# Optimization experiments

Hardware: AMD Instinct MI355X
Metric: run time of the kernel (lower is better)

## Reference

```python
import jax, jax.numpy as jnp
import numpy as np

ALPHA = 0.15
KSIZE = 5
EPS = 1e-6


def _minmax_norm(x):
    # x: [B,1,H,W]; per-sample min-max normalize, 0.5 if nearly constant
    mn = x.min(axis=(1, 2, 3), keepdims=True)
    mx = x.max(axis=(1, 2, 3), keepdims=True)
    denom = mx - mn
    safe = jnp.where(denom > EPS, denom, 1.0)
    return jnp.where(denom > EPS, (x - mn) / safe, 0.5)


def _saliency_map(images, out_hw):
    # grayscale via luma weights
    w = jnp.array([0.299, 0.587, 0.114], dtype=images.dtype).reshape(1, 3, 1, 1)
    gray = (images * w).sum(axis=1, keepdims=True)  # [B,1,H,W]
    kernel = jnp.ones((1, 1, KSIZE, KSIZE), dtype=gray.dtype) / (KSIZE * KSIZE)
    dn = ('NCHW', 'OIHW', 'NCHW')
    local_mean = jax.lax.conv_general_dilated(gray, kernel, (1, 1), 'SAME', dimension_numbers=dn)
    local_mean_sq = jax.lax.conv_general_dilated(gray ** 2, kernel, (1, 1), 'SAME', dimension_numbers=dn)
    local_var = jnp.maximum(local_mean_sq - local_mean ** 2, 0.0)
    sal = _minmax_norm(local_var)
    if sal.shape[-2:] != out_hw:
        sal = jax.image.resize(sal, (sal.shape[0], 1, out_hw[0], out_hw[1]), method='bilinear')
    return jax.lax.stop_gradient(sal)  # computed under no_grad / detached in torch


def setup_inputs() -> dict:
    key = jax.random.key(0)
    k1, k2 = jax.random.split(key)
    features = jax.random.normal(k1, (64, 512, 28, 28), dtype=jnp.float32)
    images = jax.random.uniform(k2, (64, 3, 224, 224), dtype=jnp.float32)
    return {"features": features, "images": images}


def reference(features, images):
    sal = _saliency_map(images, features.shape[-2:])  # [B,1,Hf,Wf]
    attn = jnp.sqrt((features ** 2).mean(axis=1, keepdims=True))  # [B,1,Hf,Wf]
    attn = _minmax_norm(attn)
    loss = jnp.mean((attn - sal) ** 2)
    return ALPHA * loss
```

## Files before the change

### kernel.cpp

```cpp
#include <hip/hip_runtime.h>
#include <math.h>

#define BATCH 64
#define HIMG 224
#define WIMG 224
#define IMGPLANE (HIMG*WIMG)
#define CF 512
#define HF 28
#define WF 28
#define POS (HF*WF)
#define ALPHA_C 0.15f
#define EPS_C 1e-6f

#define STRIPS 14
#define SROWS 16
#define GROWS 20
#define GCOLS 228
#define GSTR 229
#define VSTR 261
#define SHN 4580

#define NATTN 512
#define NVARH (STRIPS*BATCH)

#define OFF_HRES 0
#define HRES_CNT (BATCH*HIMG*WF)
#define OFF_BMM (OFF_HRES + HRES_CNT)
#define OFF_AP  (OFF_BMM + BATCH*STRIPS*2)
#define OFF_ACC (OFF_AP + 8*BATCH*POS)
#define OFF_CNT (OFF_ACC + 1)

__global__ __launch_bounds__(256) void fat_k(const float* __restrict__ img,
                                             const float* __restrict__ f,
                                             float* __restrict__ ws) {
    __shared__ float sh[SHN];
    __shared__ float wred[8];
    int bid = blockIdx.x;
    int tid = threadIdx.x;
    int g11 = bid / 11, r11 = bid - 11 * g11;

    if (r11 < 4) {
        int ab = g11 * 4 + r11;
        if (ab == 0 && tid == 0) {
            ws[OFF_ACC] = 0.0f;
            ((unsigned*)ws)[OFF_CNT] = 0u;
        }
        if (tid >= 196) return;
        int b = ab >> 3, z = ab & 7;
        const float* fp = f + (size_t)(b * CF + z * 64) * POS + 4 * tid;
        float ax = 0.0f, ay = 0.0f, az = 0.0f, aw = 0.0f;
        #pragma unroll 8
        for (int c = 0; c < 64; c++) {
            float4 u = *(const float4*)(fp + (size_t)c * POS);
            ax += u.x * u.x; ay += u.y * u.y; az += u.z * u.z; aw += u.w * u.w;
        }
        float4 o = make_float4(ax, ay, az, aw);
        *(float4*)(ws + OFF_AP + (size_t)(z * BATCH + b) * POS + 4 * tid) = o;
        return;
    }

    int vb = g11 * 7 + (r11 - 4);
    int b = vb / STRIPS, sy = vb - b * STRIPS;
    int y0 = sy * SROWS;
    const float* imb = img + (size_t)b * 3 * IMGPLANE;

    for (int i = tid; i < GROWS * 56; i += 256) {
        int gr = i / 56, q = i - gr * 56;
        int gy = y0 - 2 + gr;
        float gx0 = 0.0f, gx1 = 0.0f, gx2 = 0.0f, gx3 = 0.0f;
        if ((unsigned)gy < HIMG) {
            const float* row = imb + gy * WIMG + 4 * q;
            float4 a = *(const float4*)(row);
            float4 bb = *(const float4*)(row + IMGPLANE);
            float4 c = *(const float4*)(row + 2 * IMGPLANE);
            gx0 = 0.299f * a.x + 0.587f * bb.x + 0.114f * c.x;
            gx1 = 0.299f * a.y + 0.587f * bb.y + 0.114f * c.y;
            gx2 = 0.299f * a.z + 0.587f * bb.z + 0.114f * c.z;
            gx3 = 0.299f * a.w + 0.587f * bb.w + 0.114f * c.w;
        }
        int base = gr * GSTR + 2 + 4 * q;
        sh[base] = gx0; sh[base + 1] = gx1; sh[base + 2] = gx2; sh[base + 3] = gx3;
    }
    if (tid < GROWS * 4) {
        int gr = tid >> 2, p = tid & 3;
        int gc = (p < 2) ? p : (224 + p);
        sh[gr * GSTR + gc] = 0.0f;
    }
    __syncthreads();

    int r = tid >> 4, s = tid & 15;
    int x0 = 14 * s;
    const float* gr0 = sh + r * GSTR;
    float c1[5], c2[5], vreg[14];
    #pragma unroll
    for (int m = 0; m < 5; m++) {
        float a = 0.0f, a2 = 0.0f;
        #pragma unroll
        for (int k = 0; k < 5; k++) {
            float u = gr0[k * GSTR + x0 + m];
            a += u; a2 += u * u;
        }
        c1[m] = a; c2[m] = a2;
    }
    float vmn = INFINITY, vmx = 0.0f;
    #pragma unroll
    for (int xi = 0; xi < 14; xi++) {
        int p = xi % 5;
        float s1 = c1[p], s2 = c2[p];
        #pragma unroll
        for (int m = 1; m < 5; m++) {
            s1 += c1[(p + m) % 5];
            s2 += c2[(p + m) % 5];
        }
        float m1 = s1 * 0.04f, m2 = s2 * 0.04f;
        float vv = fmaxf(m2 - m1 * m1, 0.0f);
        vreg[xi] = vv;
        vmn = fminf(vmn, vv); vmx = fmaxf(vmx, vv);
        if (xi < 13) {
            float a = 0.0f, a2 = 0.0f;
            #pragma unroll
            for (int k = 0; k < 5; k++) {
                float u = gr0[k * GSTR + x0 + xi + 5];
                a += u; a2 += u * u;
            }
            c1[p] = a; c2[p] = a2;
        }
    }
    #pragma unroll
    for (int o = 32; o > 0; o >>= 1) {
        vmn = fminf(vmn, __shfl_xor(vmn, o));
        vmx = fmaxf(vmx, __shfl_xor(vmx, o));
    }
    __syncthreads();
    int w = tid >> 6;
    if ((tid & 63) == 0) { wred[w] = vmn; wred[4 + w] = vmx; }
    if (tid < SROWS * 8) {
        int rr = tid >> 3, p = tid & 7;
        int jh = p + ((p < 4) ? 0 : 224);
        sh[rr * VSTR + jh + (jh >> 3)] = 0.0f;
    }
    #pragma unroll
    for (int xi = 0; xi < 14; xi++) {
        int jh = x0 + xi + 4;
        sh[r * VSTR + jh + (jh >> 3)] = vreg[xi];
    }
    __syncthreads();
    if (tid == 0) {
        float mn = fminf(fminf(wred[0], wred[1]), fminf(wred[2], wred[3]));
        float mx = fmaxf(fmaxf(wred[4], wred[5]), fmaxf(wred[6], wred[7]));
        int blk = b * STRIPS + sy;
        ws[OFF_BMM + 2 * blk]     = mn;
        ws[OFF_BMM + 2 * blk + 1] = mx;
    }

    float* hb = ws + OFF_HRES + ((size_t)b * HIMG + y0) * WF;
    for (int idx = tid; idx < SROWS * WF; idx += 256) {
        int rr = idx / WF, i = idx - rr * WF;
        float acc = 0.0f, wsum = 0.0f;
        int j0 = 8 * i - 4;
        #pragma unroll
        for (int t = 0; t < 16; t++) {
            int j = j0 + t;
            float w_ = 8.0f - fabsf((float)t - 7.5f);
            int jh = j + 4;
            acc += w_ * sh[rr * VSTR + jh + (jh >> 3)];
            if ((unsigned)j < WIMG) wsum += w_;
        }
        hb[idx] = acc / wsum;
    }
}

__global__ __launch_bounds__(256) void fused_k(float* __restrict__ ws,
                                               float* __restrict__ out) {
    __shared__ float hres[HIMG][WF + 1];
    __shared__ float wred[4];
    __shared__ float s_mn, s_mx;
    int b = blockIdx.x;
    int tid = threadIdx.x;

    if (tid < 64) {
        float mn = INFINITY, mx = 0.0f;
        if (tid < STRIPS) {
            mn = ws[OFF_BMM + 2 * (b * STRIPS + tid)];
            mx = ws[OFF_BMM + 2 * (b * STRIPS + tid) + 1];
        }
        #pragma unroll
        for (int o = 8; o > 0; o >>= 1) {
            mn = fminf(mn, __shfl_down(mn, o));
            mx = fmaxf(mx, __shfl_down(mx, o));
        }
        if (tid == 0) { s_mn = mn; s_mx = mx; }
    }

    const float* hg = ws + OFF_HRES + (size_t)b * HIMG * WF;
    for (int i = tid; i < HIMG * WF; i += 256) {
        int y = i / WF, x = i - y * WF;
        hres[y][x] = hg[i];
    }
    __syncthreads();

    float vmn = s_mn, vmx = s_mx;
    float vden = vmx - vmn;
    bool vok = vden > EPS_C;

    const float* ap = ws + OFF_AP + (size_t)b * POS;
    float salv[4], attnv[4];
    float amn = INFINITY, amx = -INFINITY;
    #pragma unroll
    for (int k = 0; k < 4; k++) {
        int idx = tid + 256 * k;
        salv[k] = 0.0f; attnv[k] = 0.0f;
        if (idx < POS) {
            int yo = idx / WF, x = idx - yo * WF;
            float acc = 0.0f, wsum = 0.0f;
            int j0 = 8 * yo - 4;
            #pragma unroll
            for (int t = 0; t < 16; t++) {
                int j = j0 + t;
                float w = 8.0f - fabsf((float)t - 7.5f);
                if ((unsigned)j < HIMG) { acc += w * hres[j][x]; wsum += w; }
            }
            float sraw = acc / wsum;
            salv[k] = vok ? (sraw - vmn) / vden : 0.5f;
            float ssum = 0.0f;
            #pragma unroll
            for (int z = 0; z < 8; z++)
                ssum += ap[(size_t)z * BATCH * POS + idx];
            float a = sqrtf(ssum * (1.0f / CF));
            attnv[k] = a;
            amn = fminf(amn, a); amx = fmaxf(amx, a);
        }
    }

    #pragma unroll
    for (int o = 32; o > 0; o >>= 1) {
        amn = fminf(amn, __shfl_xor(amn, o));
        amx = fmaxf(amx, __shfl_xor(amx, o));
    }
    int w = tid >> 6;
    if ((tid & 63) == 0) wred[w] = amn;
    __syncthreads();
    if (tid == 0) s_mn = fminf(fminf(wred[0], wred[1]), fminf(wred[2], wred[3]));
    __syncthreads();
    if ((tid & 63) == 0) wred[w] = amx;
    __syncthreads();
    if (tid == 0) s_mx = fmaxf(fmaxf(wred[0], wred[1]), fmaxf(wred[2], wred[3]));
    __syncthreads();
    amn = s_mn; amx = s_mx;
    float aden = amx - amn;
    bool aok = aden > EPS_C;

    float lsum = 0.0f;
    #pragma unroll
    for (int k = 0; k < 4; k++) {
        int idx = tid + 256 * k;
        if (idx < POS) {
            float an = aok ? (attnv[k] - amn) / aden : 0.5f;
            float d = an - salv[k];
            lsum += d * d;
        }
    }
    #pragma unroll
    for (int o = 32; o > 0; o >>= 1) lsum += __shfl_xor(lsum, o);
    if ((tid & 63) == 0) wred[w] = lsum;
    __syncthreads();

    if (tid == 0) {
        float part = wred[0] + wred[1] + wred[2] + wred[3];
        atomicAdd(ws + OFF_ACC, part);
        __threadfence();
        unsigned old = atomicAdd((unsigned*)ws + OFF_CNT, 1u);
        if (old == BATCH - 1) {
            float tot = atomicAdd(ws + OFF_ACC, 0.0f);
            out[0] = tot * (ALPHA_C / (float)(BATCH * POS));
        }
    }
}

extern "C" void kernel_launch(void* const* d_in, const int* in_sizes, int n_in,
                              void* d_out, int out_size, void* d_ws, size_t ws_size,
                              hipStream_t stream) {
    const float* features = (const float*)d_in[0];
    const float* images   = (const float*)d_in[1];
    float* ws  = (float*)d_ws;
    float* out = (float*)d_out;

    hipLaunchKernelGGL(fat_k,   dim3(NATTN + NVARH), dim3(256), 0, stream,
                       images, features, ws);
    hipLaunchKernelGGL(fused_k, dim3(BATCH),         dim3(256), 0, stream, ws, out);
}
```

Before: 191.8 us.

## Split fused attention/variance kernel into separate launches with finer channel split

Breaks the combined kernel, which interleaved attention-reduction blocks and image-variance blocks, into two separate kernels. The channel reduction now uses 16 groups of 32 channels instead of 8 groups of 64, which doubles the attention block count to 1024, and the final kernel sums 16 partials. The aim is simpler per-block indexing and more parallelism for the feature stream. The cost is an extra launch, loss of the overlap between the two workloads, and more partial-sum traffic.

After: 193.9 us. About the same (+1.1%).

```diff
diff --git a/kernel.cpp b/kernel.cpp
--- a/kernel.cpp
+++ b/kernel.cpp
@@ -15,52 +15,47 @@
 #define STRIPS 14
 #define SROWS 16
 #define GROWS 20
-#define GCOLS 228
 #define GSTR 229
 #define VSTR 261
 #define SHN 4580
 
-#define NATTN 512
-#define NVARH (STRIPS*BATCH)
+#define ZG 16
+#define ZCH 32
 
 #define OFF_HRES 0
 #define HRES_CNT (BATCH*HIMG*WF)
 #define OFF_BMM (OFF_HRES + HRES_CNT)
 #define OFF_AP  (OFF_BMM + BATCH*STRIPS*2)
-#define OFF_ACC (OFF_AP + 8*BATCH*POS)
+#define OFF_ACC (OFF_AP + ZG*BATCH*POS)
 #define OFF_CNT (OFF_ACC + 1)
 
-__global__ __launch_bounds__(256) void fat_k(const float* __restrict__ img,
-                                             const float* __restrict__ f,
-                                             float* __restrict__ ws) {
+__global__ __launch_bounds__(256) void attn_k(const float* __restrict__ f,
+                                              float* __restrict__ ws) {
+    int z = blockIdx.x, b = blockIdx.y;
+    int tid = threadIdx.x;
+    if (z == 0 && b == 0 && tid == 0) {
+        ws[OFF_ACC] = 0.0f;
+        ((unsigned*)ws)[OFF_CNT] = 0u;
+    }
+    if (tid >= 196) return;
+    const float* fp = f + (size_t)(b * CF + z * ZCH) * POS + 4 * tid;
+    float ax = 0.0f, ay = 0.0f, az = 0.0f, aw = 0.0f;
+    #pragma unroll
+    for (int c = 0; c < ZCH; c++) {
+        float4 u = *(const float4*)(fp + (size_t)c * POS);
+        ax += u.x * u.x; ay += u.y * u.y;
+        az += u.z * u.z; aw += u.w * u.w;
+    }
+    *(float4*)(ws + OFF_AP + (size_t)(z * BATCH + b) * POS + 4 * tid) =
+        make_float4(ax, ay, az, aw);
+}
+
+__global__ __launch_bounds__(256) void varh_k(const float* __restrict__ img,
+                                              float* __restrict__ ws) {
     __shared__ float sh[SHN];
     __shared__ float wred[8];
-    int bid = blockIdx.x;
+    int sy = blockIdx.x, b = blockIdx.y;
     int tid = threadIdx.x;
-    int g11 = bid / 11, r11 = bid - 11 * g11;
-
-    if (r11 < 4) {
-        int ab = g11 * 4 + r11;
-        if (ab == 0 && tid == 0) {
-            ws[OFF_ACC] = 0.0f;
-            ((unsigned*)ws)[OFF_CNT] = 0u;
-        }
-        if (tid >= 196) return;
-        int b = ab >> 3, z = ab & 7;
-        const float* fp = f + (size_t)(b * CF + z * 64) * POS + 4 * tid;
-        float ax = 0.0f, ay = 0.0f, az = 0.0f, aw = 0.0f;
-        #pragma unroll 8
-        for (int c = 0; c < 64; c++) {
-            float4 u = *(const float4*)(fp + (size_t)c * POS);
-            ax += u.x * u.x; ay += u.y * u.y; az += u.z * u.z; aw += u.w * u.w;
-        }
-        float4 o = make_float4(ax, ay, az, aw);
-        *(float4*)(ws + OFF_AP + (size_t)(z * BATCH + b) * POS + 4 * tid) = o;
-        return;
-    }
-
-    int vb = g11 * 7 + (r11 - 4);
-    int b = vb / STRIPS, sy = vb - b * STRIPS;
     int y0 = sy * SROWS;
     const float* imb = img + (size_t)b * 3 * IMGPLANE;
 
@@ -224,7 +219,7 @@
             salv[k] = vok ? (sraw - vmn) / vden : 0.5f;
             float ssum = 0.0f;
             #pragma unroll
-            for (int z = 0; z < 8; z++)
+            for (int z = 0; z < ZG; z++)
                 ssum += ap[(size_t)z * BATCH * POS + idx];
             float a = sqrtf(ssum * (1.0f / CF));
             attnv[k] = a;
@@ -285,7 +280,7 @@
     float* ws  = (float*)d_ws;
     float* out = (float*)d_out;
 
-    hipLaunchKernelGGL(fat_k,   dim3(NATTN + NVARH), dim3(256), 0, stream,
-                       images, features, ws);
+    hipLaunchKernelGGL(attn_k,  dim3(ZG, BATCH),     dim3(256), 0, stream, features, ws);
+    hipLaunchKernelGGL(varh_k,  dim3(STRIPS, BATCH), dim3(256), 0, stream, images, ws);
     hipLaunchKernelGGL(fused_k, dim3(BATCH),         dim3(256), 0, stream, ws, out);
 }
```
